# Performance work log

Hardware: AMD Instinct MI355X
Metric: run time of the kernel (lower is better)

Reference implementation:

```python
import jax, jax.numpy as jnp
import numpy as np

LAMBDA_B = 5.0
N = 16_777_216  # 2^24 samples -> ~128 MB of fp32 inputs


def setup_inputs() -> dict:
    key = jax.random.key(0)
    k1, k2 = jax.random.split(key)
    y_true = jax.random.uniform(k1, (N,), dtype=jnp.float32)  # IWI-like scores in [0,1)
    y_pred = y_true + 0.1 * jax.random.normal(k2, (N,), dtype=jnp.float32)
    quants = jnp.arange(6, dtype=jnp.float32) / 5.0  # [0.0, 0.2, ..., 1.0]
    return {"y_pred": y_pred, "y_true": y_true, "quants": quants}


def reference(y_pred, y_true, quants):
    # MSE term
    diff = y_pred - y_true
    mse = jnp.mean(diff * diff)

    # Bucketize y_true into 5 bins: bin j is [q_j, q_{j+1}) for j<4, [q_4, q_5] for j=4.
    # searchsorted(side='right')-1 gives the half-open binning; values exactly equal
    # to quants[5] fall in the closed last bin; values outside [q0, q5] fall in no bin.
    idx = jnp.searchsorted(quants, y_true, side='right') - 1
    idx = jnp.where(y_true == quants[5], 4, idx)
    valid = (idx >= 0) & (idx <= 4)
    seg = jnp.where(valid, idx, 5).astype(jnp.int32)  # invalid -> dummy segment 5

    # Single-pass bucketized sum/count (the fused kernel this loss wants)
    sums = jax.ops.segment_sum(jnp.where(valid, diff, 0.0), seg, num_segments=6)
    counts = jax.ops.segment_sum(valid.astype(jnp.float32), seg, num_segments=6)

    bias = sums[:5] / jnp.maximum(counts[:5], 1.0)       # per-bin mean of (y_pred - y_true)
    bias2 = jnp.where(counts[:5] > 0, bias * bias, 0.0)  # empty bins contribute 0 (mask.any())
    max_bias2 = jnp.maximum(jnp.max(bias2), 0.0)         # torch starts from tensor(0.0)

    return mse + LAMBDA_B * max_bias2
```

## Files before the change

### kernel.cpp

```cpp
#include <hip/hip_runtime.h>

#define BLOCK 256
#define GRID 2048
#define FBLOCK 1024

__global__ __launch_bounds__(BLOCK) void ratledge_partial(
    const float* __restrict__ yp, const float* __restrict__ yt,
    const float* __restrict__ quants, float* __restrict__ partial, int n)
{
    float q[6];
#pragma unroll
    for (int j = 0; j < 6; ++j) q[j] = quants[j];

    float msum = 0.f;
    float bs[5] = {0.f, 0.f, 0.f, 0.f, 0.f};
    float bc[5] = {0.f, 0.f, 0.f, 0.f, 0.f};

    const int tid    = blockIdx.x * BLOCK + threadIdx.x;
    const int stride = GRID * BLOCK;
    const int n4     = n >> 2;
    const float4* yp4 = (const float4*)yp;
    const float4* yt4 = (const float4*)yt;

    for (int i = tid; i < n4; i += stride) {
        float4 p = yp4[i];
        float4 t = yt4[i];
        float pv[4] = {p.x, p.y, p.z, p.w};
        float tv[4] = {t.x, t.y, t.z, t.w};
#pragma unroll
        for (int e = 0; e < 4; ++e) {
            float v = tv[e];
            float d = pv[e] - v;
            msum = fmaf(d, d, msum);
            int cnt = 0;
#pragma unroll
            for (int j = 0; j < 6; ++j) cnt += (v >= q[j]) ? 1 : 0;
            int idx = (v == q[5]) ? 4 : (cnt - 1);
#pragma unroll
            for (int j = 0; j < 5; ++j) {
                bool m = (idx == j);
                bs[j] += m ? d   : 0.f;
                bc[j] += m ? 1.f : 0.f;
            }
        }
    }
    for (int i = (n4 << 2) + tid; i < n; i += stride) {
        float v = yt[i];
        float d = yp[i] - v;
        msum = fmaf(d, d, msum);
        int cnt = 0;
#pragma unroll
        for (int j = 0; j < 6; ++j) cnt += (v >= q[j]) ? 1 : 0;
        int idx = (v == q[5]) ? 4 : (cnt - 1);
#pragma unroll
        for (int j = 0; j < 5; ++j) {
            bool m = (idx == j);
            bs[j] += m ? d   : 0.f;
            bc[j] += m ? 1.f : 0.f;
        }
    }

    float vals[11];
    vals[0] = msum;
#pragma unroll
    for (int j = 0; j < 5; ++j) { vals[1 + j] = bs[j]; vals[6 + j] = bc[j]; }
#pragma unroll
    for (int off = 32; off > 0; off >>= 1) {
#pragma unroll
        for (int j = 0; j < 11; ++j)
            vals[j] += __shfl_down(vals[j], off, 64);
    }

    __shared__ float sred[BLOCK / 64][11];
    const int lane = threadIdx.x & 63;
    const int wid  = threadIdx.x >> 6;
    if (lane == 0) {
#pragma unroll
        for (int j = 0; j < 11; ++j) sred[wid][j] = vals[j];
    }
    __syncthreads();
    if (threadIdx.x == 0) {
#pragma unroll
        for (int j = 0; j < 11; ++j) {
            float s = sred[0][j] + sred[1][j] + sred[2][j] + sred[3][j];
            partial[j * GRID + blockIdx.x] = s;
        }
    }
}

__global__ __launch_bounds__(FBLOCK) void ratledge_final(
    const float* __restrict__ partial, float* __restrict__ out, int n)
{
    const int t    = threadIdx.x;
    const int lane = t & 63;
    const int wid  = t >> 6;

    double acc[11];
#pragma unroll
    for (int j = 0; j < 11; ++j) {
        float a0 = partial[j * GRID + t];
        float a1 = partial[j * GRID + t + FBLOCK];
        acc[j] = (double)a0 + (double)a1;
    }

#pragma unroll
    for (int off = 32; off > 0; off >>= 1) {
#pragma unroll
        for (int j = 0; j < 11; ++j)
            acc[j] += __shfl_down(acc[j], off, 64);
    }

    __shared__ double sred[FBLOCK / 64][11];
    if (lane == 0) {
#pragma unroll
        for (int j = 0; j < 11; ++j) sred[wid][j] = acc[j];
    }
    __syncthreads();

    if (wid == 0) {
        double v[11];
#pragma unroll
        for (int j = 0; j < 11; ++j)
            v[j] = (lane < FBLOCK / 64) ? sred[lane][j] : 0.0;
#pragma unroll
        for (int off = 8; off > 0; off >>= 1) {
#pragma unroll
            for (int j = 0; j < 11; ++j)
                v[j] += __shfl_down(v[j], off, 64);
        }
        if (lane == 0) {
            double mse = v[0] / (double)n;
            double maxb2 = 0.0;
#pragma unroll
            for (int j = 0; j < 5; ++j) {
                double cntj = v[6 + j];
                double bias = v[1 + j] / fmax(cntj, 1.0);
                double b2   = (cntj > 0.0) ? bias * bias : 0.0;
                maxb2 = fmax(maxb2, b2);
            }
            out[0] = (float)(mse + 5.0 * maxb2);
        }
    }
}

extern "C" void kernel_launch(void* const* d_in, const int* in_sizes, int n_in,
                              void* d_out, int out_size, void* d_ws, size_t ws_size,
                              hipStream_t stream) {
    const float* yp = (const float*)d_in[0];
    const float* yt = (const float*)d_in[1];
    const float* q  = (const float*)d_in[2];
    float* partial  = (float*)d_ws;
    float* out      = (float*)d_out;
    int n = in_sizes[0];

    ratledge_partial<<<GRID, BLOCK, 0, stream>>>(yp, yt, q, partial, n);
    ratledge_final<<<1, FBLOCK, 0, stream>>>(partial, out, n);
}
```

Baseline: 155.1 us.

## Use cumulative threshold sums per bin and batch four float4 loads per iteration

Each sample now adds into cumulative accumulators for every threshold it passes, instead of finding its bin index and doing a one-hot update. Per-bin sums and counts are recovered by differencing adjacent cumulative values in the final kernel. The grid-stride loop is also unrolled to issue four float4 loads per input before computing, which raises memory-level parallelism. Differencing large cumulative float sums can lose precision compared with direct per-bin accumulation, and the extra registers from unrolling may reduce occupancy.

Result: no change. 153.8 us (-0.8%).

```diff
diff --git a/kernel.cpp b/kernel.cpp
--- a/kernel.cpp
+++ b/kernel.cpp
@@ -1,4 +1,5 @@
 #include <hip/hip_runtime.h>
+#include <math.h>
 
 #define BLOCK 256
 #define GRID 2048
@@ -11,10 +12,11 @@
     float q[6];
 #pragma unroll
     for (int j = 0; j < 6; ++j) q[j] = quants[j];
+    const float q5 = q[5];
 
     float msum = 0.f;
-    float bs[5] = {0.f, 0.f, 0.f, 0.f, 0.f};
-    float bc[5] = {0.f, 0.f, 0.f, 0.f, 0.f};
+    float ss[5] = {0.f, 0.f, 0.f, 0.f, 0.f};
+    unsigned sc[5] = {0u, 0u, 0u, 0u, 0u};
 
     const int tid    = blockIdx.x * BLOCK + threadIdx.x;
     const int stride = GRID * BLOCK;
@@ -22,48 +24,57 @@
     const float4* yp4 = (const float4*)yp;
     const float4* yt4 = (const float4*)yt;
 
-    for (int i = tid; i < n4; i += stride) {
+    auto body = [&](float p, float v) {
+        float d = p - v;
+        msum = fmaf(d, d, msum);
+        float vv = (v <= q5) ? v : -INFINITY;
+#pragma unroll
+        for (int j = 0; j < 5; ++j) {
+            bool m = (vv >= q[j]);
+            ss[j] += m ? d : 0.f;
+            sc[j] += m ? 1u : 0u;
+        }
+    };
+
+    const int trips = n4 / stride;
+    int k = 0;
+    for (; k + 4 <= trips; k += 4) {
+        float4 P[4], T[4];
+#pragma unroll
+        for (int r = 0; r < 4; ++r) {
+            int i = tid + (k + r) * stride;
+            P[r] = yp4[i];
+            T[r] = yt4[i];
+        }
+#pragma unroll
+        for (int r = 0; r < 4; ++r) {
+            body(P[r].x, T[r].x);
+            body(P[r].y, T[r].y);
+            body(P[r].z, T[r].z);
+            body(P[r].w, T[r].w);
+        }
+    }
+    for (; k < trips; ++k) {
+        int i = tid + k * stride;
         float4 p = yp4[i];
         float4 t = yt4[i];
-        float pv[4] = {p.x, p.y, p.z, p.w};
-        float tv[4] = {t.x, t.y, t.z, t.w};
-#pragma unroll
-        for (int e = 0; e < 4; ++e) {
-            float v = tv[e];
-            float d = pv[e] - v;
-            msum = fmaf(d, d, msum);
-            int cnt = 0;
-#pragma unroll
-            for (int j = 0; j < 6; ++j) cnt += (v >= q[j]) ? 1 : 0;
-            int idx = (v == q[5]) ? 4 : (cnt - 1);
-#pragma unroll
-            for (int j = 0; j < 5; ++j) {
-                bool m = (idx == j);
-                bs[j] += m ? d   : 0.f;
-                bc[j] += m ? 1.f : 0.f;
-            }
+        body(p.x, t.x); body(p.y, t.y); body(p.z, t.z); body(p.w, t.w);
+    }
+    {
+        int i = tid + trips * stride;
+        if (i < n4) {
+            float4 p = yp4[i];
+            float4 t = yt4[i];
+            body(p.x, t.x); body(p.y, t.y); body(p.z, t.z); body(p.w, t.w);
         }
     }
-    for (int i = (n4 << 2) + tid; i < n; i += stride) {
-        float v = yt[i];
-        float d = yp[i] - v;
-        msum = fmaf(d, d, msum);
-        int cnt = 0;
-#pragma unroll
-        for (int j = 0; j < 6; ++j) cnt += (v >= q[j]) ? 1 : 0;
-        int idx = (v == q[5]) ? 4 : (cnt - 1);
-#pragma unroll
-        for (int j = 0; j < 5; ++j) {
-            bool m = (idx == j);
-            bs[j] += m ? d   : 0.f;
-            bc[j] += m ? 1.f : 0.f;
-        }
-    }
+    for (int i = (n4 << 2) + tid; i < n; i += stride)
+        body(yp[i], yt[i]);
 
     float vals[11];
     vals[0] = msum;
 #pragma unroll
-    for (int j = 0; j < 5; ++j) { vals[1 + j] = bs[j]; vals[6 + j] = bc[j]; }
+    for (int j = 0; j < 5; ++j) { vals[1 + j] = ss[j]; vals[6 + j] = (float)sc[j]; }
 #pragma unroll
     for (int off = 32; off > 0; off >>= 1) {
 #pragma unroll
@@ -133,9 +144,14 @@
             double maxb2 = 0.0;
 #pragma unroll
             for (int j = 0; j < 5; ++j) {
-                double cntj = v[6 + j];
-                double bias = v[1 + j] / fmax(cntj, 1.0);
-                double b2   = (cntj > 0.0) ? bias * bias : 0.0;
+                double Sj  = v[1 + j];
+                double Sj1 = (j < 4) ? v[2 + j] : 0.0;
+                double Cj  = v[6 + j];
+                double Cj1 = (j < 4) ? v[7 + j] : 0.0;
+                double cnt = Cj - Cj1;
+                double sum = Sj - Sj1;
+                double bias = sum / fmax(cnt, 1.0);
+                double b2   = (cnt > 0.0) ? bias * bias : 0.0;
                 maxb2 = fmax(maxb2, b2);
             }
             out[0] = (float)(mse + 5.0 * maxb2);
```
